# Performance work log

Hardware: AMD Instinct MI355X
Metric: run time of the kernel (lower is better)

## Reference

```python
import jax, jax.numpy as jnp
import numpy as np


def setup_inputs() -> dict:
    key = jax.random.key(0)
    k1, k2 = jax.random.split(key)
    z = jax.random.normal(k1, (16, 256, 32, 32), dtype=jnp.float32)
    emb = jax.random.normal(k2, (8192, 256), dtype=jnp.float32)
    return {"z": z, "emb": emb}


def reference(z, emb):
    B, C, H, W = z.shape
    # [B,C,H,W] -> [B*H*W, C], distances in fp32 for precision
    z_f = jnp.transpose(z, (0, 2, 3, 1)).reshape(-1, C).astype(jnp.float32)
    e = emb.astype(jnp.float32)
    # squared-distance expansion: ||z||^2 - 2 z.e + ||e||^2  -> [N, K]
    d = (
        jnp.sum(z_f * z_f, axis=1, keepdims=True)
        - 2.0 * (z_f @ e.T)
        + jnp.sum(e * e, axis=1)[None, :]
    )
    idx = jnp.argmin(d, axis=1)  # [N]
    out = emb[idx].astype(z.dtype)  # codebook gather
    return jnp.transpose(out.reshape(B, H, W, C), (0, 3, 1, 2))
```

## Files before the change

kernel.cpp:

```cpp
#include <hip/hip_runtime.h>
#include <stdint.h>

#define NB   16
#define CD   256
#define HW   1024
#define NQ   16384
#define KCN  8192

typedef unsigned long long u64;
typedef unsigned short     u16;
using f32x4  = __attribute__((ext_vector_type(4))) float;
using bf16x8 = __attribute__((ext_vector_type(8))) __bf16;

#define ZT_OFF   0
#define ZTB_OFF  16777216
#define EMBB_OFF 25165824
#define EH_OFF   29360128
#define CAND_OFF 29392896
#define IDX_OFF  37781504

static __device__ __forceinline__ void gl_lds16(const void* g, void* l) {
  __builtin_amdgcn_global_load_lds(
      (const __attribute__((address_space(1))) void*)g,
      (__attribute__((address_space(3))) void*)l, 16, 0, 0);
}

static __device__ __forceinline__ unsigned bf16r(float x) {
  unsigned u = __float_as_uint(x);
  return (u + 0x7fffu + ((u >> 16) & 1u)) >> 16;
}

static __device__ __forceinline__ u64 umin64(u64 a, u64 b) { return a < b ? a : b; }
static __device__ __forceinline__ u64 umax64(u64 a, u64 b) { return a < b ? b : a; }

__global__ __launch_bounds__(256) void k_prep(const float* __restrict__ z,
                                              const float* __restrict__ emb,
                                              float* __restrict__ zT,
                                              u16* __restrict__ zTb,
                                              u16* __restrict__ embB,
                                              float* __restrict__ eH) {
  const int bx = (int)blockIdx.x;
  if (bx < 1024) {
    __shared__ float tile[64][65];
    const int b   = bx >> 6;
    const int hwT = (bx >> 2) & 15;
    const int cT  = bx & 3;
    const int tx  = threadIdx.x & 63;
    const int ty  = threadIdx.x >> 6;
    const float* src = z + (size_t)(b * CD + cT * 64) * HW + hwT * 64;
#pragma unroll
    for (int i = 0; i < 16; ++i) {
      const int c_l = ty + 4 * i;
      tile[c_l][tx] = src[(size_t)c_l * HW + tx];
    }
    __syncthreads();
    const size_t dbase = (size_t)(b * HW + hwT * 64) * CD + cT * 64;
#pragma unroll
    for (int i = 0; i < 16; ++i) {
      const int hw_l = ty + 4 * i;
      const float v = tile[tx][hw_l];
      zT [dbase + (size_t)hw_l * CD + tx] = v;
      zTb[dbase + (size_t)hw_l * CD + tx] = (u16)bf16r(v);
    }
  } else {
    const int wave = (bx - 1024) * 4 + ((int)threadIdx.x >> 6);
    const int lane = threadIdx.x & 63;
#pragma unroll
    for (int it = 0; it < 8; ++it) {
      const int row = wave * 8 + it;
      const float4 v = *(const float4*)(emb + (size_t)row * CD + lane * 4);
      uint2 pk;
      pk.x = bf16r(v.x) | (bf16r(v.y) << 16);
      pk.y = bf16r(v.z) | (bf16r(v.w) << 16);
      *(uint2*)(embB + (size_t)row * CD + lane * 4) = pk;
      float s = v.x * v.x + v.y * v.y + v.z * v.z + v.w * v.w;
#pragma unroll
      for (int off = 32; off; off >>= 1) s += __shfl_xor(s, off, 64);
      if (lane == 0) eH[row] = 0.5f * s + 1024.0f;
    }
  }
}

#define NT  4
#define BKC 4

__global__ __launch_bounds__(256, 2) void k_argmin(const u16* __restrict__ zTb,
                                                   const u16* __restrict__ embB,
                                                   const float* __restrict__ eH,
                                                   u64* __restrict__ cand) {
  __shared__ __align__(16) u16 As[128 * 64];
  __shared__ __align__(16) u16 Bs[128 * 64];
  const int tid  = threadIdx.x;
  const int w    = tid >> 6;
  const int lane = tid & 63;
  const int l15  = lane & 15, quad = lane >> 4, l7 = lane & 7;
  const int q0    = (int)(blockIdx.x >> 4) * 128;
  const int split = (int)(blockIdx.x & 15);
  const int wq0 = (w & 1) * 64, wn0 = (w >> 1) * 64, wh = w >> 1;

  const int srow  = w * 32 + (lane >> 3);
  const int scol8 = (l7 ^ (lane >> 3)) * 8;
  const int ldsL  = w * 4096 + lane * 16;
  const int co0 = ((0 * 4 + quad) ^ l7) * 16;
  const int co1 = ((1 * 4 + quad) ^ l7) * 16;

  u64 b1[16], b2[16];
#pragma unroll
  for (int s = 0; s < 16; ++s) { b1[s] = ~0ull; b2[s] = ~0ull; }

  for (int nt = 0; nt < NT; ++nt) {
    const int n0 = split * 512 + nt * 128;
    float eh[4];
#pragma unroll
    for (int j = 0; j < 4; ++j) eh[j] = eH[n0 + wn0 + 16 * j + l15];

    f32x4 acc[4][4];
#pragma unroll
    for (int i = 0; i < 4; ++i)
#pragma unroll
      for (int j = 0; j < 4; ++j) acc[i][j] = f32x4{0.f, 0.f, 0.f, 0.f};

    for (int kc = 0; kc < BKC; ++kc) {
#pragma unroll
      for (int i = 0; i < 4; ++i) {
        const int row = srow + i * 8;
        gl_lds16(zTb  + (size_t)(q0 + row) * CD + kc * 64 + scol8,
                 (char*)As + ldsL + i * 1024);
        gl_lds16(embB + (size_t)(n0 + row) * CD + kc * 64 + scol8,
                 (char*)Bs + ldsL + i * 1024);
      }
      __syncthreads();
#pragma unroll
      for (int ks = 0; ks < 2; ++ks) {
        const int co = ks ? co1 : co0;
        bf16x8 af[4], bfr[4];
#pragma unroll
        for (int i = 0; i < 4; ++i)
          af[i] = *(const bf16x8*)((const char*)As + (wq0 + i * 16 + l15) * 128 + co);
#pragma unroll
        for (int j = 0; j < 4; ++j)
          bfr[j] = *(const bf16x8*)((const char*)Bs + (wn0 + j * 16 + l15) * 128 + co);
#pragma unroll
        for (int i = 0; i < 4; ++i)
#pragma unroll
          for (int j = 0; j < 4; ++j)
            acc[i][j] = __builtin_amdgcn_mfma_f32_16x16x32_bf16(af[i], bfr[j],
                                                                acc[i][j], 0, 0, 0);
      }
      __syncthreads();
    }
    const unsigned nl = (unsigned)(n0 + wn0 + l15);
#pragma unroll
    for (int i = 0; i < 4; ++i) {
#pragma unroll
      for (int r = 0; r < 4; ++r) {
        const int s = i * 4 + r;
        const u64 p0 = ((u64)__float_as_uint(eh[0] - acc[i][0][r]) << 32) | (nl);
        const u64 p1 = ((u64)__float_as_uint(eh[1] - acc[i][1][r]) << 32) | (nl + 16);
        const u64 p2 = ((u64)__float_as_uint(eh[2] - acc[i][2][r]) << 32) | (nl + 32);
        const u64 p3 = ((u64)__float_as_uint(eh[3] - acc[i][3][r]) << 32) | (nl + 48);
        const u64 lo01 = umin64(p0, p1), hi01 = umax64(p0, p1);
        const u64 lo23 = umin64(p2, p3), hi23 = umax64(p2, p3);
        const u64 best = umin64(lo01, lo23);
        const u64 sec  = umin64(umax64(lo01, lo23), umin64(hi01, hi23));
        const u64 nb2  = umin64(umax64(best, b1[s]), umin64(sec, b2[s]));
        b1[s] = umin64(best, b1[s]);
        b2[s] = nb2;
      }
    }
  }
#pragma unroll
  for (int s = 0; s < 16; ++s) {
    u64 x1 = b1[s], x2 = b2[s];
#pragma unroll
    for (int off = 1; off < 16; off <<= 1) {
      const u64 o1 = __shfl_xor(x1, off, 64);
      const u64 o2 = __shfl_xor(x2, off, 64);
      const u64 lo = umin64(x1, o1);
      const u64 hi = umax64(x1, o1);
      x1 = lo;
      x2 = umin64(hi, umin64(x2, o2));
    }
    if (l15 == 0) {
      const int i = s >> 2, r = s & 3;
      const int q = q0 + wq0 + i * 16 + quad * 4 + r;
      cand[(size_t)q * 64 + split * 4 + wh * 2 + 0] = x1;
      cand[(size_t)q * 64 + split * 4 + wh * 2 + 1] = x2;
    }
  }
}

__global__ __launch_bounds__(256) void k_pick(const float* __restrict__ zT,
                                              const float* __restrict__ emb,
                                              const u64* __restrict__ cand,
                                              int* __restrict__ idxF) {
  const int lane = threadIdx.x & 63;
  const int wv   = threadIdx.x >> 6;
  const int sub  = lane >> 4;
  const int l15  = lane & 15;
  const int q = (int)(blockIdx.x * 16) + wv * 4 + sub;

  u64 s0 = ~0ull, s1 = ~0ull, s2 = ~0ull, s3 = ~0ull;
  const u64* cp = cand + (size_t)q * 64 + l15 * 4;
#pragma unroll
  for (int j = 0; j < 4; ++j) {
    u64 v = cp[j];
    const u64 t0 = umin64(s0, v); v = umax64(s0, v); s0 = t0;
    const u64 t1 = umin64(s1, v); v = umax64(s1, v); s1 = t1;
    const u64 t2 = umin64(s2, v); v = umax64(s2, v); s2 = t2;
    s3 = umin64(s3, v);
  }
#pragma unroll
  for (int off = 1; off < 16; off <<= 1) {
    const u64 b0 = __shfl_xor(s0, off, 64);
    const u64 b1 = __shfl_xor(s1, off, 64);
    const u64 b2 = __shfl_xor(s2, off, 64);
    const u64 b3 = __shfl_xor(s3, off, 64);
    const u64 c0 = umin64(s0, b0);
    const u64 c1 = umin64(umin64(s1, b1), umax64(s0, b0));
    const u64 c2 = umin64(umin64(s2, b2),
                          umin64(umax64(s1, b0), umax64(s0, b1)));
    const u64 c3 = umin64(umin64(umin64(s3, b3), umax64(s2, b0)),
                          umin64(umax64(s0, b2), umax64(s1, b1)));
    s0 = c0; s1 = c1; s2 = c2; s3 = c3;
  }
  const u64 sel[4] = {s0, s1, s2, s3};

  const float* zrow = zT + (size_t)q * CD + l15 * 16;
  const float4 za = *(const float4*)(zrow + 0);
  const float4 zb = *(const float4*)(zrow + 4);
  const float4 zc = *(const float4*)(zrow + 8);
  const float4 zd = *(const float4*)(zrow + 12);
  double bd = 1e300;
  int bi = 0x7fffffff;
#pragma unroll
  for (int t = 0; t < 4; ++t) {
    const int idx = (int)(unsigned)(sel[t] & 0xffffffffull);
    const float* er = emb + (size_t)idx * CD + l15 * 16;
    const float4 ea = *(const float4*)(er + 0);
    const float4 eb = *(const float4*)(er + 4);
    const float4 ec = *(const float4*)(er + 8);
    const float4 ed = *(const float4*)(er + 12);
    double s = 0.0;
#define ACC1(zv, ev) { const double d = (double)(zv) - (double)(ev); s += d * d; }
    ACC1(za.x, ea.x) ACC1(za.y, ea.y) ACC1(za.z, ea.z) ACC1(za.w, ea.w)
    ACC1(zb.x, eb.x) ACC1(zb.y, eb.y) ACC1(zb.z, eb.z) ACC1(zb.w, eb.w)
    ACC1(zc.x, ec.x) ACC1(zc.y, ec.y) ACC1(zc.z, ec.z) ACC1(zc.w, ec.w)
    ACC1(zd.x, ed.x) ACC1(zd.y, ed.y) ACC1(zd.z, ed.z) ACC1(zd.w, ed.w)
#undef ACC1
#pragma unroll
    for (int off = 1; off < 16; off <<= 1) s += __shfl_xor(s, off, 64);
    if (s < bd || (s == bd && idx < bi)) { bd = s; bi = idx; }
  }
  if (l15 == 0) idxF[q] = bi;
}

__global__ __launch_bounds__(256) void k_gather(const float* __restrict__ emb,
                                                const int* __restrict__ idxF,
                                                float* __restrict__ out) {
  const int b   = (int)(blockIdx.x >> 4);
  const int hw0 = (int)(blockIdx.x & 15) * 64;
  const int lane = threadIdx.x & 63;
  const int cg   = threadIdx.x >> 6;
  const int hw = hw0 + lane;
  const int k  = idxF[b * HW + hw];
  const float* er = emb + (size_t)k * CD + cg * 64;
  float* ob = out + (size_t)b * CD * HW + (size_t)(cg * 64) * HW + hw;
#pragma unroll
  for (int j = 0; j < 16; ++j) {
    const float4 e = *(const float4*)(er + j * 4);
    ob[(size_t)(j * 4 + 0) * HW] = e.x;
    ob[(size_t)(j * 4 + 1) * HW] = e.y;
    ob[(size_t)(j * 4 + 2) * HW] = e.z;
    ob[(size_t)(j * 4 + 3) * HW] = e.w;
  }
}

extern "C" void kernel_launch(void* const* d_in, const int* in_sizes, int n_in,
                              void* d_out, int out_size, void* d_ws, size_t ws_size,
                              hipStream_t stream) {
  const float* z   = (const float*)d_in[0];
  const float* emb = (const float*)d_in[1];
  float* out = (float*)d_out;

  char* ws = (char*)d_ws;
  float* zT   = (float*)(ws + ZT_OFF);
  u16*   zTb  = (u16*)(ws + ZTB_OFF);
  u16*   embB = (u16*)(ws + EMBB_OFF);
  float* eH   = (float*)(ws + EH_OFF);
  u64*   cand = (u64*)(ws + CAND_OFF);
  int*   idxF = (int*)(ws + IDX_OFF);

  k_prep<<<1280, 256, 0, stream>>>(z, emb, zT, zTb, embB, eH);
  k_argmin<<<2048, 256, 0, stream>>>(zTb, embB, eH, cand);
  k_pick<<<1024, 256, 0, stream>>>(zT, emb, cand, idxF);
  k_gather<<<256, 256, 0, stream>>>(emb, idxF, out);
}
```

Before: 203.1 us.

## Pack candidate keys into fp32, halve codebook splits, fuse pick with gather

The argmin kernel now gives each block 1024 codes instead of 512, halving the grid and the candidate buffer. The running top-2 is tracked with float min/max on keys whose low 5 mantissa bits carry the tile and column index, replacing 64-bit compare chains. The lane index is restored before the cross-lane reduction and the full code index is rebuilt at write time. The pick kernel now writes the output directly through an LDS transpose, removing the separate gather kernel and the index buffer, but truncating 5 mantissa bits coarsens the ranking used for candidate selection.

```diff
diff --git a/kernel.cpp b/kernel.cpp
--- a/kernel.cpp
+++ b/kernel.cpp
@@ -17,7 +17,6 @@
 #define EMBB_OFF 25165824
 #define EH_OFF   29360128
 #define CAND_OFF 29392896
-#define IDX_OFF  37781504
 
 static __device__ __forceinline__ void gl_lds16(const void* g, void* l) {
   __builtin_amdgcn_global_load_lds(
@@ -81,7 +80,7 @@
   }
 }
 
-#define NT  4
+#define NT  8
 #define BKC 4
 
 __global__ __launch_bounds__(256, 2) void k_argmin(const u16* __restrict__ zTb,
@@ -94,8 +93,8 @@
   const int w    = tid >> 6;
   const int lane = tid & 63;
   const int l15  = lane & 15, quad = lane >> 4, l7 = lane & 7;
-  const int q0    = (int)(blockIdx.x >> 4) * 128;
-  const int split = (int)(blockIdx.x & 15);
+  const int q0    = (int)(blockIdx.x >> 3) * 128;
+  const int split = (int)(blockIdx.x & 7);
   const int wq0 = (w & 1) * 64, wn0 = (w >> 1) * 64, wh = w >> 1;
 
   const int srow  = w * 32 + (lane >> 3);
@@ -104,12 +103,13 @@
   const int co0 = ((0 * 4 + quad) ^ l7) * 16;
   const int co1 = ((1 * 4 + quad) ^ l7) * 16;
 
-  u64 b1[16], b2[16];
-#pragma unroll
-  for (int s = 0; s < 16; ++s) { b1[s] = ~0ull; b2[s] = ~0ull; }
+  const float FMAX = __uint_as_float(0x7F7FFFFFu);
+  float b1[16], b2[16];
+#pragma unroll
+  for (int s = 0; s < 16; ++s) { b1[s] = FMAX; b2[s] = FMAX; }
 
   for (int nt = 0; nt < NT; ++nt) {
-    const int n0 = split * 512 + nt * 128;
+    const int n0 = split * 1024 + nt * 128;
     float eh[4];
 #pragma unroll
     for (int j = 0; j < 4; ++j) eh[j] = eH[n0 + wn0 + 16 * j + l15];
@@ -149,29 +149,31 @@
       }
       __syncthreads();
     }
-    const unsigned nl = (unsigned)(n0 + wn0 + l15);
 #pragma unroll
     for (int i = 0; i < 4; ++i) {
 #pragma unroll
       for (int r = 0; r < 4; ++r) {
         const int s = i * 4 + r;
-        const u64 p0 = ((u64)__float_as_uint(eh[0] - acc[i][0][r]) << 32) | (nl);
-        const u64 p1 = ((u64)__float_as_uint(eh[1] - acc[i][1][r]) << 32) | (nl + 16);
-        const u64 p2 = ((u64)__float_as_uint(eh[2] - acc[i][2][r]) << 32) | (nl + 32);
-        const u64 p3 = ((u64)__float_as_uint(eh[3] - acc[i][3][r]) << 32) | (nl + 48);
-        const u64 lo01 = umin64(p0, p1), hi01 = umax64(p0, p1);
-        const u64 lo23 = umin64(p2, p3), hi23 = umax64(p2, p3);
-        const u64 best = umin64(lo01, lo23);
-        const u64 sec  = umin64(umax64(lo01, lo23), umin64(hi01, hi23));
-        const u64 nb2  = umin64(umax64(best, b1[s]), umin64(sec, b2[s]));
-        b1[s] = umin64(best, b1[s]);
-        b2[s] = nb2;
+        float kq[4];
+#pragma unroll
+        for (int j = 0; j < 4; ++j) {
+          const unsigned kb = (__float_as_uint(eh[j] - acc[i][j][r]) & ~31u)
+                              | (unsigned)(nt * 4 + j);
+          kq[j] = __uint_as_float(kb);
+        }
+        const float lo01 = fminf(kq[0], kq[1]), hi01 = fmaxf(kq[0], kq[1]);
+        const float lo23 = fminf(kq[2], kq[3]), hi23 = fmaxf(kq[2], kq[3]);
+        const float best = fminf(lo01, lo23);
+        const float sec  = fminf(fmaxf(lo01, lo23), fminf(hi01, hi23));
+        b2[s] = fminf(fmaxf(best, b1[s]), fminf(sec, b2[s]));
+        b1[s] = fminf(best, b1[s]);
       }
     }
   }
 #pragma unroll
   for (int s = 0; s < 16; ++s) {
-    u64 x1 = b1[s], x2 = b2[s];
+    u64 x1 = ((u64)__float_as_uint(b1[s]) << 32) | (unsigned)l15;
+    u64 x2 = ((u64)__float_as_uint(b2[s]) << 32) | (unsigned)l15;
 #pragma unroll
     for (int off = 1; off < 16; off <<= 1) {
       const u64 o1 = __shfl_xor(x1, off, 64);
@@ -184,32 +186,33 @@
     if (l15 == 0) {
       const int i = s >> 2, r = s & 3;
       const int q = q0 + wq0 + i * 16 + quad * 4 + r;
-      cand[(size_t)q * 64 + split * 4 + wh * 2 + 0] = x1;
-      cand[(size_t)q * 64 + split * 4 + wh * 2 + 1] = x2;
-    }
-  }
-}
-
-__global__ __launch_bounds__(256) void k_pick(const float* __restrict__ zT,
-                                              const float* __restrict__ emb,
-                                              const u64* __restrict__ cand,
-                                              int* __restrict__ idxF) {
+      const unsigned kb1 = (unsigned)(x1 >> 32), kb2 = (unsigned)(x2 >> 32);
+      const int n1 = split * 1024 + (int)((kb1 >> 2) & 7) * 128 + wn0
+                     + 16 * (int)(kb1 & 3) + (int)(x1 & 15);
+      const int n2 = split * 1024 + (int)((kb2 >> 2) & 7) * 128 + wn0
+                     + 16 * (int)(kb2 & 3) + (int)(x2 & 15);
+      cand[(size_t)q * 32 + split * 4 + wh * 2 + 0] = ((u64)kb1 << 32) | (unsigned)n1;
+      cand[(size_t)q * 32 + split * 4 + wh * 2 + 1] = ((u64)kb2 << 32) | (unsigned)n2;
+    }
+  }
+}
+
+__global__ __launch_bounds__(256) void k_pick_out(const float* __restrict__ zT,
+                                                  const float* __restrict__ emb,
+                                                  const u64* __restrict__ cand,
+                                                  float* __restrict__ out) {
+  __shared__ float tile[16][257];
   const int lane = threadIdx.x & 63;
   const int wv   = threadIdx.x >> 6;
   const int sub  = lane >> 4;
   const int l15  = lane & 15;
-  const int q = (int)(blockIdx.x * 16) + wv * 4 + sub;
-
-  u64 s0 = ~0ull, s1 = ~0ull, s2 = ~0ull, s3 = ~0ull;
-  const u64* cp = cand + (size_t)q * 64 + l15 * 4;
-#pragma unroll
-  for (int j = 0; j < 4; ++j) {
-    u64 v = cp[j];
-    const u64 t0 = umin64(s0, v); v = umax64(s0, v); s0 = t0;
-    const u64 t1 = umin64(s1, v); v = umax64(s1, v); s1 = t1;
-    const u64 t2 = umin64(s2, v); v = umax64(s2, v); s2 = t2;
-    s3 = umin64(s3, v);
-  }
+  const int q0b  = (int)blockIdx.x * 16;
+  const int q    = q0b + wv * 4 + sub;
+  const int hwl  = wv * 4 + sub;
+
+  const u64* cp = cand + (size_t)q * 32 + l15 * 2;
+  const u64 v0 = cp[0], v1 = cp[1];
+  u64 s0 = umin64(v0, v1), s1 = umax64(v0, v1), s2 = ~0ull, s3 = ~0ull;
 #pragma unroll
   for (int off = 1; off < 16; off <<= 1) {
     const u64 b0 = __shfl_xor(s0, off, 64);
@@ -252,27 +255,28 @@
     for (int off = 1; off < 16; off <<= 1) s += __shfl_xor(s, off, 64);
     if (s < bd || (s == bd && idx < bi)) { bd = s; bi = idx; }
   }
-  if (l15 == 0) idxF[q] = bi;
-}
-
-__global__ __launch_bounds__(256) void k_gather(const float* __restrict__ emb,
-                                                const int* __restrict__ idxF,
-                                                float* __restrict__ out) {
-  const int b   = (int)(blockIdx.x >> 4);
-  const int hw0 = (int)(blockIdx.x & 15) * 64;
-  const int lane = threadIdx.x & 63;
-  const int cg   = threadIdx.x >> 6;
-  const int hw = hw0 + lane;
-  const int k  = idxF[b * HW + hw];
-  const float* er = emb + (size_t)k * CD + cg * 64;
-  float* ob = out + (size_t)b * CD * HW + (size_t)(cg * 64) * HW + hw;
-#pragma unroll
-  for (int j = 0; j < 16; ++j) {
-    const float4 e = *(const float4*)(er + j * 4);
-    ob[(size_t)(j * 4 + 0) * HW] = e.x;
-    ob[(size_t)(j * 4 + 1) * HW] = e.y;
-    ob[(size_t)(j * 4 + 2) * HW] = e.z;
-    ob[(size_t)(j * 4 + 3) * HW] = e.w;
+  {
+    const float* er = emb + (size_t)bi * CD + l15 * 16;
+    const float4 ea = *(const float4*)(er + 0);
+    const float4 eb = *(const float4*)(er + 4);
+    const float4 ec = *(const float4*)(er + 8);
+    const float4 ed = *(const float4*)(er + 12);
+    *(float4*)&tile[hwl][l15 * 16 + 0]  = ea;
+    *(float4*)&tile[hwl][l15 * 16 + 4]  = eb;
+    *(float4*)&tile[hwl][l15 * 16 + 8]  = ec;
+    *(float4*)&tile[hwl][l15 * 16 + 12] = ed;
+  }
+  __syncthreads();
+  const int t = threadIdx.x;
+  const int b = q0b >> 10, hw0 = q0b & 1023;
+  float* optr = out + (size_t)b * CD * HW + (size_t)t * HW + hw0;
+  float v[16];
+#pragma unroll
+  for (int j = 0; j < 16; ++j) v[j] = tile[j][t];
+#pragma unroll
+  for (int m = 0; m < 4; ++m) {
+    float4 f; f.x = v[4 * m]; f.y = v[4 * m + 1]; f.z = v[4 * m + 2]; f.w = v[4 * m + 3];
+    *(float4*)(optr + 4 * m) = f;
   }
 }
 
@@ -289,10 +293,8 @@
   u16*   embB = (u16*)(ws + EMBB_OFF);
   float* eH   = (float*)(ws + EH_OFF);
   u64*   cand = (u64*)(ws + CAND_OFF);
-  int*   idxF = (int*)(ws + IDX_OFF);
 
   k_prep<<<1280, 256, 0, stream>>>(z, emb, zT, zTb, embB, eH);
-  k_argmin<<<2048, 256, 0, stream>>>(zTb, embB, eH, cand);
-  k_pick<<<1024, 256, 0, stream>>>(zT, emb, cand, idxF);
-  k_gather<<<256, 256, 0, stream>>>(emb, idxF, out);
-}
+  k_argmin<<<1024, 256, 0, stream>>>(zTb, embB, eH, cand);
+  k_pick_out<<<1024, 256, 0, stream>>>(zT, emb, cand, out);
+}
```

After: 186.3 us. -8.3%, faster.
